# Optimization experiments

Measured on AMD Instinct MI355X. Metric: run time of the kernel, lower is better.

The kernel has to match this reference:

```python
import jax, jax.numpy as jnp
import numpy as np

SIGMA = 2.0      # test_cfg.sigma (gaussian kernel)
MASK_THR = 0.5   # test_cfg.mask_thr
NUM_CLASSES = 80


def setup_inputs() -> dict:
    key = jax.random.key(0)
    k1, k2, k3 = jax.random.split(key, 3)
    N, H, W = 500, 200, 304  # nms_pre instances, mask-feat resolution (stride-4 of 800x1216)
    mask_preds = jax.random.uniform(k1, (N, H, W), dtype=jnp.float32)
    labels = jax.random.randint(k2, (N,), 0, NUM_CLASSES, dtype=jnp.int32)
    scores = jax.random.uniform(k3, (N,), dtype=jnp.float32)
    return {"mask_preds": mask_preds, "labels": labels, "scores": scores}


def reference(mask_preds, labels, scores):
    """Matrix NMS (gaussian kernel) as in mask_matrix_nms with filter_thr=-1, max_num=-1.

    mask_preds: (N, H, W) sigmoid probabilities; thresholded at MASK_THR to binary masks
    labels:     (N,) int32 class ids
    scores:     (N,) float32 classification scores
    Returns (scores, labels, masks, keep_inds) with fixed shape N.
    """
    N = scores.shape[0]
    masks = (mask_preds > MASK_THR).astype(jnp.float32)           # (N,H,W) binary
    mask_area = masks.sum((1, 2))                                  # (N,)

    # sort by score, descending
    order = jnp.argsort(-scores)
    scores_s = scores[order]
    masks_s = masks[order]
    area_s = mask_area[order]
    labels_s = labels[order]

    flat = masks_s.reshape(N, -1)                                  # (N, H*W)
    inter = flat @ flat.T                                          # (N,N) intersection
    union = area_s[:, None] + area_s[None, :] - inter
    iou = jnp.triu(inter / union, k=1)                             # (N,N) upper-tri IoU

    label_eq = jnp.triu((labels_s[:, None] == labels_s[None, :]).astype(jnp.float32), k=1)
    decay_iou = iou * label_eq                                     # same-class IoU

    compensate_iou = decay_iou.max(axis=0)                         # (N,) max IoU w/ higher-scored same-class mask
    decay_matrix = jnp.exp(-SIGMA * decay_iou ** 2)                # (N,N)
    compensate_matrix = jnp.exp(-SIGMA * compensate_iou ** 2)[:, None]  # broadcast along rows (torch transpose)
    decay_coefficient = (decay_matrix / compensate_matrix).min(axis=0)  # (N,)

    scores_decayed = scores_s * decay_coefficient

    # final sort by decayed score, descending
    order2 = jnp.argsort(-scores_decayed)
    out_scores = scores_decayed[order2]
    out_labels = labels_s[order2]
    out_masks = masks_s[order2]
    keep_inds = order[order2]
    return out_scores, out_labels, out_masks, keep_inds
```

## Files before the change

kernel.cpp:

```cpp
#include <hip/hip_runtime.h>

typedef unsigned long long ull;
typedef float f32x4 __attribute__((ext_vector_type(4)));

constexpr int N   = 500;
constexpr int HW  = 60800;
constexpr int NW  = 950;
constexpr int NC  = 80;
constexpr int NTILES = N * NW / 4;
constexpr int PB  = 1024;
constexpr int IOUB = 256;
constexpr int QPB = (HW / 4 + 255) / 256;

__global__ void __launch_bounds__(512)
k_packsort(const float* __restrict__ mp, const int* __restrict__ labels,
           const float* __restrict__ scores,
           ull* __restrict__ packed, int* __restrict__ order_g,
           float* __restrict__ scoresS_g, int* __restrict__ labelsS_g,
           int* __restrict__ offs_g, int* __restrict__ members_g,
           int2* __restrict__ pairList, int* __restrict__ counters) {
    const int t    = threadIdx.x;
    const int lane = t & 63;

    if (blockIdx.x != 0) {
        int wid = (blockIdx.x - 1) * 8 + (t >> 6);
        for (int tile = wid; tile < NTILES; tile += PB * 8) {
            size_t base = (size_t)tile * 256;
            float v0 = mp[base +   0 + lane];
            float v1 = mp[base +  64 + lane];
            float v2 = mp[base + 128 + lane];
            float v3 = mp[base + 192 + lane];
            ull b0 = __ballot(v0 > 0.5f);
            ull b1 = __ballot(v1 > 0.5f);
            ull b2 = __ballot(v2 > 0.5f);
            ull b3 = __ballot(v3 > 0.5f);
            if (lane == 0) {
                longlong4 w;
                w.x = (long long)b0; w.y = (long long)b1;
                w.z = (long long)b2; w.w = (long long)b3;
                *(longlong4*)(packed + tile * 4) = w;
            }
        }
        return;
    }

    __shared__ float sS[N];
    __shared__ int   orderS[N];
    __shared__ int   labS[N];
    __shared__ int   cnt[NC];
    __shared__ int   offs[NC + 1];
    __shared__ int   members[N];
    __shared__ int   pcnt;

    if (t == 0) { counters[0] = 0; pcnt = 0; }
    if (t < N) sS[t] = scores[t];
    if (t < NC) cnt[t] = 0;
    __syncthreads();
    if (t < N) {
        float si = sS[t];
        int rank = 0;
        for (int j = 0; j < N; ++j) {
            float sj = sS[j];
            if (sj > si || (sj == si && j < t)) rank++;
        }
        orderS[rank] = t;
    }
    __syncthreads();
    int myLab = -1;
    if (t < N) {
        int o = orderS[t];
        order_g[t]   = o;
        scoresS_g[t] = sS[o];
        myLab = labels[o];
        labS[t] = myLab;
        labelsS_g[t] = myLab;
    }
    __syncthreads();
    if (t < N) atomicAdd(&cnt[myLab], 1);
    __syncthreads();
    if (t == 0) {
        int s = 0;
        for (int c = 0; c < NC; ++c) { offs[c] = s; s += cnt[c]; }
        offs[NC] = s;
    }
    __syncthreads();
    if (t < NC) cnt[t] = offs[t];
    __syncthreads();
    if (t < N) { int p = atomicAdd(&cnt[myLab], 1); members[p] = t; }
    __syncthreads();
    if (t < NC) {
        int b = offs[t], e = offs[t + 1];
        for (int a = b; a < e; ++a)
            for (int c2 = a + 1; c2 < e; ++c2) {
                int i = members[a], j = members[c2];
                int lo = min(i, j), hi = max(i, j);
                int p = atomicAdd(&pcnt, 1);
                pairList[p] = make_int2(lo, hi);
            }
    }
    __syncthreads();
    if (t <= NC) offs_g[t] = offs[t];
    if (t < N)   members_g[t] = members[t];
    if (t == 0)  counters[1] = pcnt;
}

__global__ void __launch_bounds__(512)
k_ioudecay(const ull* __restrict__ packed, const int* __restrict__ order_g,
           const float* __restrict__ scoresS_g, const int* __restrict__ labelsS_g,
           const int* __restrict__ offs_g, const int* __restrict__ members_g,
           const int2* __restrict__ pairList, int* __restrict__ counters,
           int* __restrict__ iouI, int* __restrict__ keepOrig_g,
           float* __restrict__ outScores, float* __restrict__ outLabels,
           float* __restrict__ outKeep) {
    const int t    = threadIdx.x;
    const int lane = t & 63;
    __shared__ int sLast;

    int np = counters[1];
    for (int p = (int)blockIdx.x * 8 + (t >> 6); p < np; p += IOUB * 8) {
        int2 pr = pairList[p];
        const ull* A = packed + (size_t)order_g[pr.x] * NW;
        const ull* B = packed + (size_t)order_g[pr.y] * NW;
        ull acc = 0;
        for (int w = lane; w < NW; w += 64) {
            ull a = A[w], b = B[w];
            acc += (ull)__popcll(a & b)
                 + ((ull)__popcll(a) << 21)
                 + ((ull)__popcll(b) << 42);
        }
#pragma unroll
        for (int off = 32; off > 0; off >>= 1) acc += __shfl_down(acc, off, 64);
        if (lane == 0) {
            float inter = (float)(int)(acc & 0x1FFFFF);
            float areaA = (float)(int)((acc >> 21) & 0x1FFFFF);
            float areaB = (float)(int)((acc >> 42) & 0x1FFFFF);
            float uni   = areaA + areaB - inter;
            __hip_atomic_store(iouI + pr.x * N + pr.y,
                               __float_as_int(inter / uni),
                               __ATOMIC_RELAXED, __HIP_MEMORY_SCOPE_AGENT);
        }
    }
    asm volatile("s_waitcnt vmcnt(0)" ::: "memory");
    __syncthreads();
    if (t == 0) sLast = __hip_atomic_fetch_add(counters, 1, __ATOMIC_RELAXED,
                                               __HIP_MEMORY_SCOPE_AGENT);
    __syncthreads();
    if (sLast != IOUB - 1) return;

    __shared__ int   labS[N];
    __shared__ float compS[N];
    __shared__ float sdec[N];
    __shared__ int   offs[NC + 1];
    __shared__ int   members[N];
    if (t < N)  { labS[t] = labelsS_g[t]; members[t] = members_g[t]; }
    if (t <= NC) offs[t] = offs_g[t];
    __syncthreads();
    if (t < N) {
        int lj = labS[t];
        float m = 0.f;
        int b = offs[lj], e = offs[lj + 1];
        for (int q = b; q < e; ++q) {
            int i = members[q];
            if (i < t) {
                float v = __int_as_float(__hip_atomic_load(
                    iouI + i * N + t, __ATOMIC_RELAXED, __HIP_MEMORY_SCOPE_AGENT));
                m = fmaxf(m, v);
            }
        }
        compS[t] = m;
    }
    __syncthreads();
    if (t < N) {
        int lj = labS[t];
        float c = 1.f;
        int b = offs[lj], e = offs[lj + 1];
        for (int q = b; q < e; ++q) {
            int i = members[q];
            if (i < t) {
                float d = __int_as_float(__hip_atomic_load(
                    iouI + i * N + t, __ATOMIC_RELAXED, __HIP_MEMORY_SCOPE_AGENT));
                float ci = compS[i];
                c = fminf(c, expf(-2.f * d * d) / expf(-2.f * ci * ci));
            }
        }
        sdec[t] = scoresS_g[t] * c;
    }
    __syncthreads();
    if (t < N) {
        float sj = sdec[t];
        int rank = 0;
        for (int i = 0; i < N; ++i) {
            float si = sdec[i];
            if (si > sj || (si == sj && i < t)) rank++;
        }
        int o = order_g[t];
        outScores[rank]  = sj;
        outLabels[rank]  = (float)labS[t];
        outKeep[rank]    = (float)o;
        keepOrig_g[rank] = o;
    }
}

__global__ void k_gather(const ull* __restrict__ packed, const int* __restrict__ keepOrig,
                         f32x4* __restrict__ outMasks) {
    int q = blockIdx.x * blockDim.x + threadIdx.x;
    if (q >= HW / 4) return;
    int k    = blockIdx.y;
    int orig = keepOrig[k];
    ull w  = packed[(size_t)orig * NW + (q >> 4)];
    int sh = (q & 15) * 4;
    f32x4 r;
    r.x = (float)((w >> (sh    )) & 1ULL);
    r.y = (float)((w >> (sh + 1)) & 1ULL);
    r.z = (float)((w >> (sh + 2)) & 1ULL);
    r.w = (float)((w >> (sh + 3)) & 1ULL);
    outMasks[(size_t)k * (HW / 4) + q] = r;
}

extern "C" void kernel_launch(void* const* d_in, const int* in_sizes, int n_in,
                              void* d_out, int out_size, void* d_ws, size_t ws_size,
                              hipStream_t stream) {
    const float* mask_preds = (const float*)d_in[0];
    const int*   labels     = (const int*)d_in[1];
    const float* scores     = (const float*)d_in[2];

    float*  o         = (float*)d_out;
    float*  outScores = o;
    float*  outLabels = o + N;
    f32x4*  outMasks  = (f32x4*)(o + 2 * N);
    float*  outKeep   = o + 2 * N + (size_t)N * HW;

    char* w = (char*)d_ws;
    ull*   packed     = (ull*)w;   w += (size_t)N * NW * 8;
    int*   order_g    = (int*)w;   w += N * 4;
    float* scoresS_g  = (float*)w; w += N * 4;
    int*   labelsS_g  = (int*)w;   w += N * 4;
    int*   offs_g     = (int*)w;   w += (NC + 4) * 4;
    int*   members_g  = (int*)w;   w += N * 4;
    int*   keepOrig_g = (int*)w;   w += N * 4;
    int*   counters   = (int*)w;   w += 128;
    int*   iouI       = (int*)w;   w += (size_t)N * N * 4;
    int2*  pairList   = (int2*)w;

    hipLaunchKernelGGL(k_packsort, dim3(PB + 1), dim3(512), 0, stream,
                       mask_preds, labels, scores, packed, order_g,
                       scoresS_g, labelsS_g, offs_g, members_g, pairList, counters);
    hipLaunchKernelGGL(k_ioudecay, dim3(IOUB), dim3(512), 0, stream,
                       packed, order_g, scoresS_g, labelsS_g, offs_g, members_g,
                       pairList, counters, iouI, keepOrig_g,
                       outScores, outLabels, outKeep);
    hipLaunchKernelGGL(k_gather, dim3(QPB, N), dim3(256), 0, stream,
                       packed, keepOrig_g, outMasks);
}
```

Measured before the change: 82.53 us.

## Fuse pack/sort and IoU-decay kernels with a device-wide ticket barrier

Merges the packing/sorting kernel and the IoU/decay kernel into one launch. The last-arriving blocks (by atomic ticket) spin until all blocks finish packing, then do the pairwise IoU and the final decay and sort. The aim is to remove one kernel launch and its inter-kernel gap. In exchange it adds a spin barrier that only works if the last IOUB ticketed blocks are co-resident, relaxed agent-scope stores for visibility, and a memset launch to zero the counters.

After: 101.3 us. +22.7%, slower.

```diff
diff --git a/kernel.cpp b/kernel.cpp
--- a/kernel.cpp
+++ b/kernel.cpp
@@ -9,18 +9,33 @@
 constexpr int NC  = 80;
 constexpr int NTILES = N * NW / 4;
 constexpr int PB  = 1024;
+constexpr int G   = PB + 1;
 constexpr int IOUB = 256;
 constexpr int QPB = (HW / 4 + 255) / 256;
 
+__device__ __forceinline__ void st_agent(int* p, int v) {
+    __hip_atomic_store(p, v, __ATOMIC_RELAXED, __HIP_MEMORY_SCOPE_AGENT);
+}
+__device__ __forceinline__ void st_agent_f(float* p, float v) {
+    __hip_atomic_store(p, v, __ATOMIC_RELAXED, __HIP_MEMORY_SCOPE_AGENT);
+}
+__device__ __forceinline__ void st_agent_u64(ull* p, ull v) {
+    __hip_atomic_store(p, v, __ATOMIC_RELAXED, __HIP_MEMORY_SCOPE_AGENT);
+}
+
 __global__ void __launch_bounds__(512)
-k_packsort(const float* __restrict__ mp, const int* __restrict__ labels,
-           const float* __restrict__ scores,
-           ull* __restrict__ packed, int* __restrict__ order_g,
-           float* __restrict__ scoresS_g, int* __restrict__ labelsS_g,
-           int* __restrict__ offs_g, int* __restrict__ members_g,
-           int2* __restrict__ pairList, int* __restrict__ counters) {
+k_fused(const float* __restrict__ mp, const int* __restrict__ labels,
+        const float* __restrict__ scores,
+        ull* __restrict__ packed, int* __restrict__ order_g,
+        float* __restrict__ scoresS_g, int* __restrict__ labelsS_g,
+        int* __restrict__ offs_g, int* __restrict__ members_g,
+        ull* __restrict__ pairList, int* __restrict__ counters,
+        int* __restrict__ iouI, int* __restrict__ keepOrig_g,
+        float* __restrict__ outScores, float* __restrict__ outLabels,
+        float* __restrict__ outKeep) {
     const int t    = threadIdx.x;
     const int lane = t & 63;
+    __shared__ int sTicket;
 
     if (blockIdx.x != 0) {
         int wid = (blockIdx.x - 1) * 8 + (t >> 6);
@@ -35,92 +50,94 @@
             ull b2 = __ballot(v2 > 0.5f);
             ull b3 = __ballot(v3 > 0.5f);
             if (lane == 0) {
-                longlong4 w;
-                w.x = (long long)b0; w.y = (long long)b1;
-                w.z = (long long)b2; w.w = (long long)b3;
-                *(longlong4*)(packed + tile * 4) = w;
-            }
-        }
-        return;
-    }
-
-    __shared__ float sS[N];
-    __shared__ int   orderS[N];
-    __shared__ int   labS[N];
-    __shared__ int   cnt[NC];
-    __shared__ int   offs[NC + 1];
-    __shared__ int   members[N];
-    __shared__ int   pcnt;
-
-    if (t == 0) { counters[0] = 0; pcnt = 0; }
-    if (t < N) sS[t] = scores[t];
-    if (t < NC) cnt[t] = 0;
-    __syncthreads();
-    if (t < N) {
-        float si = sS[t];
-        int rank = 0;
-        for (int j = 0; j < N; ++j) {
-            float sj = sS[j];
-            if (sj > si || (sj == si && j < t)) rank++;
-        }
-        orderS[rank] = t;
-    }
-    __syncthreads();
-    int myLab = -1;
-    if (t < N) {
-        int o = orderS[t];
-        order_g[t]   = o;
-        scoresS_g[t] = sS[o];
-        myLab = labels[o];
-        labS[t] = myLab;
-        labelsS_g[t] = myLab;
-    }
-    __syncthreads();
-    if (t < N) atomicAdd(&cnt[myLab], 1);
-    __syncthreads();
+                st_agent_u64(packed + tile * 4 + 0, b0);
+                st_agent_u64(packed + tile * 4 + 1, b1);
+                st_agent_u64(packed + tile * 4 + 2, b2);
+                st_agent_u64(packed + tile * 4 + 3, b3);
+            }
+        }
+    } else {
+        __shared__ float sS[N];
+        __shared__ int   orderS[N];
+        __shared__ int   labS[N];
+        __shared__ int   cnt[NC];
+        __shared__ int   offs[NC + 1];
+        __shared__ int   members[N];
+        __shared__ int   pcnt;
+        if (t == 0) pcnt = 0;
+        if (t < N) sS[t] = scores[t];
+        if (t < NC) cnt[t] = 0;
+        __syncthreads();
+        if (t < N) {
+            float si = sS[t];
+            int rank = 0;
+            for (int j = 0; j < N; ++j) {
+                float sj = sS[j];
+                if (sj > si || (sj == si && j < t)) rank++;
+            }
+            orderS[rank] = t;
+        }
+        __syncthreads();
+        int myLab = -1;
+        if (t < N) {
+            int o = orderS[t];
+            st_agent(order_g + t, o);
+            st_agent_f(scoresS_g + t, sS[o]);
+            myLab = labels[o];
+            labS[t] = myLab;
+            st_agent(labelsS_g + t, myLab);
+        }
+        __syncthreads();
+        if (t < N) atomicAdd(&cnt[myLab], 1);
+        __syncthreads();
+        if (t == 0) {
+            int s = 0;
+            for (int c = 0; c < NC; ++c) { offs[c] = s; s += cnt[c]; }
+            offs[NC] = s;
+        }
+        __syncthreads();
+        if (t < NC) cnt[t] = offs[t];
+        __syncthreads();
+        if (t < N) { int p = atomicAdd(&cnt[myLab], 1); members[p] = t; }
+        __syncthreads();
+        if (t < NC) {
+            int b = offs[t], e = offs[t + 1];
+            for (int a = b; a < e; ++a)
+                for (int c2 = a + 1; c2 < e; ++c2) {
+                    int i = members[a], j = members[c2];
+                    ull lo = (ull)min(i, j), hi = (ull)max(i, j);
+                    int p = atomicAdd(&pcnt, 1);
+                    st_agent_u64(pairList + p, lo | (hi << 32));
+                }
+        }
+        __syncthreads();
+        if (t <= NC) st_agent(offs_g + t, offs[t]);
+        if (t < N)   st_agent(members_g + t, members[t]);
+        if (t == 0)  st_agent(counters + 2, pcnt);
+    }
+
+    asm volatile("s_waitcnt vmcnt(0)" ::: "memory");
+    __syncthreads();
+    if (t == 0) sTicket = __hip_atomic_fetch_add(counters, 1, __ATOMIC_RELAXED,
+                                                 __HIP_MEMORY_SCOPE_AGENT);
+    __syncthreads();
+    int role = sTicket - (G - IOUB);
+    if (role < 0) return;
     if (t == 0) {
-        int s = 0;
-        for (int c = 0; c < NC; ++c) { offs[c] = s; s += cnt[c]; }
-        offs[NC] = s;
-    }
-    __syncthreads();
-    if (t < NC) cnt[t] = offs[t];
-    __syncthreads();
-    if (t < N) { int p = atomicAdd(&cnt[myLab], 1); members[p] = t; }
-    __syncthreads();
-    if (t < NC) {
-        int b = offs[t], e = offs[t + 1];
-        for (int a = b; a < e; ++a)
-            for (int c2 = a + 1; c2 < e; ++c2) {
-                int i = members[a], j = members[c2];
-                int lo = min(i, j), hi = max(i, j);
-                int p = atomicAdd(&pcnt, 1);
-                pairList[p] = make_int2(lo, hi);
-            }
-    }
-    __syncthreads();
-    if (t <= NC) offs_g[t] = offs[t];
-    if (t < N)   members_g[t] = members[t];
-    if (t == 0)  counters[1] = pcnt;
-}
-
-__global__ void __launch_bounds__(512)
-k_ioudecay(const ull* __restrict__ packed, const int* __restrict__ order_g,
-           const float* __restrict__ scoresS_g, const int* __restrict__ labelsS_g,
-           const int* __restrict__ offs_g, const int* __restrict__ members_g,
-           const int2* __restrict__ pairList, int* __restrict__ counters,
-           int* __restrict__ iouI, int* __restrict__ keepOrig_g,
-           float* __restrict__ outScores, float* __restrict__ outLabels,
-           float* __restrict__ outKeep) {
-    const int t    = threadIdx.x;
-    const int lane = t & 63;
-    __shared__ int sLast;
-
-    int np = counters[1];
-    for (int p = (int)blockIdx.x * 8 + (t >> 6); p < np; p += IOUB * 8) {
-        int2 pr = pairList[p];
-        const ull* A = packed + (size_t)order_g[pr.x] * NW;
-        const ull* B = packed + (size_t)order_g[pr.y] * NW;
+        while (__hip_atomic_load(counters, __ATOMIC_RELAXED,
+                                 __HIP_MEMORY_SCOPE_AGENT) < G)
+            __builtin_amdgcn_s_sleep(8);
+    }
+    __syncthreads();
+    asm volatile("" ::: "memory");
+
+    int np = __hip_atomic_load(counters + 2, __ATOMIC_RELAXED,
+                               __HIP_MEMORY_SCOPE_AGENT);
+    for (int p = role * 8 + (t >> 6); p < np; p += IOUB * 8) {
+        ull pr = pairList[p];
+        int px = (int)(pr & 0xFFFFFFFF), py = (int)(pr >> 32);
+        const ull* A = packed + (size_t)order_g[px] * NW;
+        const ull* B = packed + (size_t)order_g[py] * NW;
         ull acc = 0;
         for (int w = lane; w < NW; w += 64) {
             ull a = A[w], b = B[w];
@@ -135,69 +152,69 @@
             float areaA = (float)(int)((acc >> 21) & 0x1FFFFF);
             float areaB = (float)(int)((acc >> 42) & 0x1FFFFF);
             float uni   = areaA + areaB - inter;
-            __hip_atomic_store(iouI + pr.x * N + pr.y,
-                               __float_as_int(inter / uni),
-                               __ATOMIC_RELAXED, __HIP_MEMORY_SCOPE_AGENT);
+            st_agent(iouI + px * N + py, __float_as_int(inter / uni));
         }
     }
     asm volatile("s_waitcnt vmcnt(0)" ::: "memory");
     __syncthreads();
-    if (t == 0) sLast = __hip_atomic_fetch_add(counters, 1, __ATOMIC_RELAXED,
-                                               __HIP_MEMORY_SCOPE_AGENT);
-    __syncthreads();
-    if (sLast != IOUB - 1) return;
-
-    __shared__ int   labS[N];
-    __shared__ float compS[N];
-    __shared__ float sdec[N];
-    __shared__ int   offs[NC + 1];
-    __shared__ int   members[N];
-    if (t < N)  { labS[t] = labelsS_g[t]; members[t] = members_g[t]; }
-    if (t <= NC) offs[t] = offs_g[t];
-    __syncthreads();
-    if (t < N) {
-        int lj = labS[t];
-        float m = 0.f;
-        int b = offs[lj], e = offs[lj + 1];
-        for (int q = b; q < e; ++q) {
-            int i = members[q];
-            if (i < t) {
-                float v = __int_as_float(__hip_atomic_load(
-                    iouI + i * N + t, __ATOMIC_RELAXED, __HIP_MEMORY_SCOPE_AGENT));
-                m = fmaxf(m, v);
-            }
-        }
-        compS[t] = m;
-    }
-    __syncthreads();
-    if (t < N) {
-        int lj = labS[t];
-        float c = 1.f;
-        int b = offs[lj], e = offs[lj + 1];
-        for (int q = b; q < e; ++q) {
-            int i = members[q];
-            if (i < t) {
-                float d = __int_as_float(__hip_atomic_load(
-                    iouI + i * N + t, __ATOMIC_RELAXED, __HIP_MEMORY_SCOPE_AGENT));
-                float ci = compS[i];
-                c = fminf(c, expf(-2.f * d * d) / expf(-2.f * ci * ci));
-            }
-        }
-        sdec[t] = scoresS_g[t] * c;
-    }
-    __syncthreads();
-    if (t < N) {
-        float sj = sdec[t];
-        int rank = 0;
-        for (int i = 0; i < N; ++i) {
-            float si = sdec[i];
-            if (si > sj || (si == sj && i < t)) rank++;
-        }
-        int o = order_g[t];
-        outScores[rank]  = sj;
-        outLabels[rank]  = (float)labS[t];
-        outKeep[rank]    = (float)o;
-        keepOrig_g[rank] = o;
+    if (t == 0) sTicket = __hip_atomic_fetch_add(counters + 1, 1, __ATOMIC_RELAXED,
+                                                 __HIP_MEMORY_SCOPE_AGENT);
+    __syncthreads();
+    if (sTicket != IOUB - 1) return;
+
+    {
+        __shared__ int   labS[N];
+        __shared__ float compS[N];
+        __shared__ float sdec[N];
+        __shared__ int   offs[NC + 1];
+        __shared__ int   members[N];
+        if (t < N)  { labS[t] = labelsS_g[t]; members[t] = members_g[t]; }
+        if (t <= NC) offs[t] = offs_g[t];
+        __syncthreads();
+        if (t < N) {
+            int lj = labS[t];
+            float m = 0.f;
+            int b = offs[lj], e = offs[lj + 1];
+            for (int q = b; q < e; ++q) {
+                int i = members[q];
+                if (i < t) {
+                    float v = __int_as_float(__hip_atomic_load(
+                        iouI + i * N + t, __ATOMIC_RELAXED, __HIP_MEMORY_SCOPE_AGENT));
+                    m = fmaxf(m, v);
+                }
+            }
+            compS[t] = m;
+        }
+        __syncthreads();
+        if (t < N) {
+            int lj = labS[t];
+            float c = 1.f;
+            int b = offs[lj], e = offs[lj + 1];
+            for (int q = b; q < e; ++q) {
+                int i = members[q];
+                if (i < t) {
+                    float d = __int_as_float(__hip_atomic_load(
+                        iouI + i * N + t, __ATOMIC_RELAXED, __HIP_MEMORY_SCOPE_AGENT));
+                    float ci = compS[i];
+                    c = fminf(c, expf(-2.f * d * d) / expf(-2.f * ci * ci));
+                }
+            }
+            sdec[t] = scoresS_g[t] * c;
+        }
+        __syncthreads();
+        if (t < N) {
+            float sj = sdec[t];
+            int rank = 0;
+            for (int i = 0; i < N; ++i) {
+                float si = sdec[i];
+                if (si > sj || (si == sj && i < t)) rank++;
+            }
+            int o = order_g[t];
+            outScores[rank]  = sj;
+            outLabels[rank]  = (float)labS[t];
+            outKeep[rank]    = (float)o;
+            keepOrig_g[rank] = o;
+        }
     }
 }
 
@@ -240,14 +257,14 @@
     int*   keepOrig_g = (int*)w;   w += N * 4;
     int*   counters   = (int*)w;   w += 128;
     int*   iouI       = (int*)w;   w += (size_t)N * N * 4;
-    int2*  pairList   = (int2*)w;
-
-    hipLaunchKernelGGL(k_packsort, dim3(PB + 1), dim3(512), 0, stream,
+    ull*   pairList   = (ull*)w;
+
+    (void)hipMemsetAsync(counters, 0, 128, stream);
+
+    hipLaunchKernelGGL(k_fused, dim3(G), dim3(512), 0, stream,
                        mask_preds, labels, scores, packed, order_g,
-                       scoresS_g, labelsS_g, offs_g, members_g, pairList, counters);
-    hipLaunchKernelGGL(k_ioudecay, dim3(IOUB), dim3(512), 0, stream,
-                       packed, order_g, scoresS_g, labelsS_g, offs_g, members_g,
-                       pairList, counters, iouI, keepOrig_g,
+                       scoresS_g, labelsS_g, offs_g, members_g, pairList,
+                       counters, iouI, keepOrig_g,
                        outScores, outLabels, outKeep);
     hipLaunchKernelGGL(k_gather, dim3(QPB, N), dim3(256), 0, stream,
                        packed, keepOrig_g, outMasks);
```

## Store IoU per pair compactly and reduce decay via LDS atomics

Applied to the files above, without the earlier changes.

IoUs are now written to a compact per-pair array instead of a scattered N×N matrix. The final block streams the pair list in chunks through shared memory and computes the compensate max and decay min with LDS atomicMax/atomicMin on float bit patterns. This replaces per-thread serial scans over class members, which had uneven lengths and uncoalesced global loads. The cost is two extra passes over the pair list plus LDS atomic contention. The bit-pattern min/max is only valid because the values are non-negative.

After: 78.23 us. 5.2% less time.

```diff
diff --git a/kernel.cpp b/kernel.cpp
--- a/kernel.cpp
+++ b/kernel.cpp
@@ -11,13 +11,13 @@
 constexpr int PB  = 1024;
 constexpr int IOUB = 256;
 constexpr int QPB = (HW / 4 + 255) / 256;
+constexpr int CHUNK = 3072;
 
 __global__ void __launch_bounds__(512)
 k_packsort(const float* __restrict__ mp, const int* __restrict__ labels,
            const float* __restrict__ scores,
            ull* __restrict__ packed, int* __restrict__ order_g,
            float* __restrict__ scoresS_g, int* __restrict__ labelsS_g,
-           int* __restrict__ offs_g, int* __restrict__ members_g,
            int2* __restrict__ pairList, int* __restrict__ counters) {
     const int t    = threadIdx.x;
     const int lane = t & 63;
@@ -99,17 +99,14 @@
             }
     }
     __syncthreads();
-    if (t <= NC) offs_g[t] = offs[t];
-    if (t < N)   members_g[t] = members[t];
     if (t == 0)  counters[1] = pcnt;
 }
 
 __global__ void __launch_bounds__(512)
 k_ioudecay(const ull* __restrict__ packed, const int* __restrict__ order_g,
            const float* __restrict__ scoresS_g, const int* __restrict__ labelsS_g,
-           const int* __restrict__ offs_g, const int* __restrict__ members_g,
            const int2* __restrict__ pairList, int* __restrict__ counters,
-           int* __restrict__ iouI, int* __restrict__ keepOrig_g,
+           int* __restrict__ iouC, int* __restrict__ keepOrig_g,
            float* __restrict__ outScores, float* __restrict__ outLabels,
            float* __restrict__ outKeep) {
     const int t    = threadIdx.x;
@@ -135,8 +132,7 @@
             float areaA = (float)(int)((acc >> 21) & 0x1FFFFF);
             float areaB = (float)(int)((acc >> 42) & 0x1FFFFF);
             float uni   = areaA + areaB - inter;
-            __hip_atomic_store(iouI + pr.x * N + pr.y,
-                               __float_as_int(inter / uni),
+            __hip_atomic_store(iouC + p, __float_as_int(inter / uni),
                                __ATOMIC_RELAXED, __HIP_MEMORY_SCOPE_AGENT);
         }
     }
@@ -148,43 +144,47 @@
     if (sLast != IOUB - 1) return;
 
     __shared__ int   labS[N];
-    __shared__ float compS[N];
+    __shared__ int   compB[N];
+    __shared__ int   coefB[N];
     __shared__ float sdec[N];
-    __shared__ int   offs[NC + 1];
-    __shared__ int   members[N];
-    if (t < N)  { labS[t] = labelsS_g[t]; members[t] = members_g[t]; }
-    if (t <= NC) offs[t] = offs_g[t];
-    __syncthreads();
-    if (t < N) {
-        int lj = labS[t];
-        float m = 0.f;
-        int b = offs[lj], e = offs[lj + 1];
-        for (int q = b; q < e; ++q) {
-            int i = members[q];
-            if (i < t) {
-                float v = __int_as_float(__hip_atomic_load(
-                    iouI + i * N + t, __ATOMIC_RELAXED, __HIP_MEMORY_SCOPE_AGENT));
-                m = fmaxf(m, v);
-            }
-        }
-        compS[t] = m;
-    }
-    __syncthreads();
-    if (t < N) {
-        int lj = labS[t];
-        float c = 1.f;
-        int b = offs[lj], e = offs[lj + 1];
-        for (int q = b; q < e; ++q) {
-            int i = members[q];
-            if (i < t) {
-                float d = __int_as_float(__hip_atomic_load(
-                    iouI + i * N + t, __ATOMIC_RELAXED, __HIP_MEMORY_SCOPE_AGENT));
-                float ci = compS[i];
-                c = fminf(c, expf(-2.f * d * d) / expf(-2.f * ci * ci));
-            }
-        }
-        sdec[t] = scoresS_g[t] * c;
-    }
+    __shared__ int2  pch[CHUNK];
+    __shared__ float ich[CHUNK];
+
+    if (t < N) {
+        labS[t]  = labelsS_g[t];
+        compB[t] = 0;
+        coefB[t] = 0x3F800000;
+    }
+    __syncthreads();
+    for (int base = 0; base < np; base += CHUNK) {
+        int n = min(np - base, CHUNK);
+        for (int u = t; u < n; u += 512) {
+            pch[u] = pairList[base + u];
+            ich[u] = __int_as_float(__hip_atomic_load(
+                iouC + base + u, __ATOMIC_RELAXED, __HIP_MEMORY_SCOPE_AGENT));
+        }
+        __syncthreads();
+        for (int u = t; u < n; u += 512)
+            atomicMax(&compB[pch[u].y], __float_as_int(ich[u]));
+        __syncthreads();
+    }
+    for (int base = 0; base < np; base += CHUNK) {
+        int n = min(np - base, CHUNK);
+        for (int u = t; u < n; u += 512) {
+            pch[u] = pairList[base + u];
+            ich[u] = __int_as_float(__hip_atomic_load(
+                iouC + base + u, __ATOMIC_RELAXED, __HIP_MEMORY_SCOPE_AGENT));
+        }
+        __syncthreads();
+        for (int u = t; u < n; u += 512) {
+            float d  = ich[u];
+            float ci = __int_as_float(compB[pch[u].x]);
+            float r  = expf(-2.f * d * d) / expf(-2.f * ci * ci);
+            atomicMin(&coefB[pch[u].y], __float_as_int(r));
+        }
+        __syncthreads();
+    }
+    if (t < N) sdec[t] = scoresS_g[t] * __int_as_float(coefB[t]);
     __syncthreads();
     if (t < N) {
         float sj = sdec[t];
@@ -235,19 +235,17 @@
     int*   order_g    = (int*)w;   w += N * 4;
     float* scoresS_g  = (float*)w; w += N * 4;
     int*   labelsS_g  = (int*)w;   w += N * 4;
-    int*   offs_g     = (int*)w;   w += (NC + 4) * 4;
-    int*   members_g  = (int*)w;   w += N * 4;
     int*   keepOrig_g = (int*)w;   w += N * 4;
     int*   counters   = (int*)w;   w += 128;
-    int*   iouI       = (int*)w;   w += (size_t)N * N * 4;
+    int*   iouC       = (int*)w;   w += (size_t)(N * (N - 1) / 2) * 4;
     int2*  pairList   = (int2*)w;
 
     hipLaunchKernelGGL(k_packsort, dim3(PB + 1), dim3(512), 0, stream,
                        mask_preds, labels, scores, packed, order_g,
-                       scoresS_g, labelsS_g, offs_g, members_g, pairList, counters);
+                       scoresS_g, labelsS_g, pairList, counters);
     hipLaunchKernelGGL(k_ioudecay, dim3(IOUB), dim3(512), 0, stream,
-                       packed, order_g, scoresS_g, labelsS_g, offs_g, members_g,
-                       pairList, counters, iouI, keepOrig_g,
+                       packed, order_g, scoresS_g, labelsS_g,
+                       pairList, counters, iouC, keepOrig_g,
                        outScores, outLabels, outKeep);
     hipLaunchKernelGGL(k_gather, dim3(QPB, N), dim3(256), 0, stream,
                        packed, keepOrig_g, outMasks);
```
